# Optimization experiments

Hardware: AMD Instinct MI355X
Metric: run time of the kernel (lower is better)

The kernel has to match this reference:

```python
import jax, jax.numpy as jnp
import numpy as np

DIM = 32
NUM_FEATURES = 16
NUM_GRAPHS = 64
EDGE_HID = 64


def setup_inputs() -> dict:
    key = jax.random.key(0)
    ks = jax.random.split(key, 24)
    N, E = 25000, 250000
    p = lambda k, shape: (jax.random.normal(k, shape, dtype=jnp.float32) * 0.05)
    return {
        "x": jax.random.normal(ks[0], (N, NUM_FEATURES), dtype=jnp.float32),
        "edge_index": jax.random.randint(ks[1], (2, E), 0, N, dtype=jnp.int32),
        "edge_attr": jax.random.uniform(ks[2], (E, 5), dtype=jnp.float32),
        "batch": jnp.sort(jax.random.randint(ks[3], (N,), 0, NUM_GRAPHS, dtype=jnp.int32)),
        "lin0_w": p(ks[4], (NUM_FEATURES, DIM)),
        "lin0_b": p(ks[5], (DIM,)),
        "mlp_w1": p(ks[6], (5, EDGE_HID)),
        "mlp_b1": p(ks[7], (EDGE_HID,)),
        "mlp_w2": p(ks[8], (EDGE_HID, DIM * DIM)),
        "mlp_b2": p(ks[9], (DIM * DIM,)),
        "conv_bias": p(ks[10], (DIM,)),
        "gru_w_ih": p(ks[11], (3 * DIM, DIM)),
        "gru_w_hh": p(ks[12], (3 * DIM, DIM)),
        "gru_b_ih": p(ks[13], (3 * DIM,)),
        "gru_b_hh": p(ks[14], (3 * DIM,)),
        "lstm_w_ih": p(ks[15], (4 * DIM, 2 * DIM)),
        "lstm_w_hh": p(ks[16], (4 * DIM, DIM)),
        "lstm_b_ih": p(ks[17], (4 * DIM,)),
        "lstm_b_hh": p(ks[18], (4 * DIM,)),
    }


def reference(x, edge_index, edge_attr, batch, lin0_w, lin0_b, mlp_w1, mlp_b1,
              mlp_w2, mlp_b2, conv_bias, gru_w_ih, gru_w_hh, gru_b_ih, gru_b_hh,
              lstm_w_ih, lstm_w_hh, lstm_b_ih, lstm_b_hh):
    N = x.shape[0]
    src, dst = edge_index[0], edge_index[1]

    # lin0 + relu
    out = jax.nn.relu(x @ lin0_w + lin0_b)  # [N, D]
    h = out

    # edge MLP -> per-edge [D, D] weight matrices (edge_attr is loop-invariant)
    ew = jax.nn.relu(edge_attr @ mlp_w1 + mlp_b1) @ mlp_w2 + mlp_b2
    W = ew.reshape(-1, DIM, DIM)  # [E, D, D]

    deg = jax.ops.segment_sum(jnp.ones_like(dst, dtype=x.dtype), dst, num_segments=N)
    deg = jnp.maximum(deg, 1.0)[:, None]

    feat_last = out
    for _ in range(3):
        # NNConv: gather, per-edge matmul, scatter-mean, bias, relu
        msg = jnp.einsum('ei,eio->eo', out[src], W)  # [E, D]
        agg = jax.ops.segment_sum(msg, dst, num_segments=N) / deg
        m = jax.nn.relu(agg + conv_bias)
        # GRU step (torch GRU gate order r, z, n)
        gi = m @ gru_w_ih.T + gru_b_ih
        gh = h @ gru_w_hh.T + gru_b_hh
        ir, iz, inn = jnp.split(gi, 3, axis=-1)
        hr, hz, hn = jnp.split(gh, 3, axis=-1)
        r = jax.nn.sigmoid(ir + hr)
        z = jax.nn.sigmoid(iz + hz)
        n = jnp.tanh(inn + r * hn)
        h = (1.0 - z) * n + z * h
        out = h
        feat_last = out

    # Set2Set pooling (3 processing steps), LSTM input 2D hidden D
    B = NUM_GRAPHS
    q_star = jnp.zeros((B, 2 * DIM), dtype=x.dtype)
    hh = jnp.zeros((B, DIM), dtype=x.dtype)
    cc = jnp.zeros((B, DIM), dtype=x.dtype)
    for _ in range(3):
        gates = q_star @ lstm_w_ih.T + lstm_b_ih + hh @ lstm_w_hh.T + lstm_b_hh
        gi_, gf_, gg_, go_ = jnp.split(gates, 4, axis=-1)
        i_ = jax.nn.sigmoid(gi_)
        f_ = jax.nn.sigmoid(gf_)
        g_ = jnp.tanh(gg_)
        o_ = jax.nn.sigmoid(go_)
        cc = f_ * cc + i_ * g_
        hh = o_ * jnp.tanh(cc)
        q = hh  # [B, D]
        e = jnp.sum(out * q[batch], axis=-1)  # [N]
        emax = jax.ops.segment_max(e, batch, num_segments=B)
        e2 = jnp.exp(e - emax[batch])
        denom = jax.ops.segment_sum(e2, batch, num_segments=B)
        a = e2 / denom[batch]
        r_pool = jax.ops.segment_sum(a[:, None] * out, batch, num_segments=B)
        q_star = jnp.concatenate([q, r_pool], axis=-1)  # [B, 2D]

    return (q_star, feat_last)
```

## Files before the change

kernel.cpp:

```cpp
#include <hip/hip_runtime.h>
#include <hip/hip_fp16.h>

#define NFEAT 16
#define D 32
#define NB 64
#define TCOLS 2080
#define CHUNK 8
#define CPAD 16
#define KBN 16

static inline size_t align_up(size_t x, size_t a){ return (x + a - 1) & ~(a - 1); }

typedef _Float16 f16x2 __attribute__((ext_vector_type(2)));
typedef _Float16 f16x8 __attribute__((ext_vector_type(8)));
typedef float f32x4 __attribute__((ext_vector_type(4)));

__device__ inline unsigned int pk2(float a, float b){
  __half2 h = __floats2half2_rn(a, b);
  union { __half2 h; unsigned int u; } cv; cv.h = h; return cv.u;
}

__device__ inline float dot2(unsigned int a, unsigned int b, float c){
  union { unsigned int u; f16x2 h; } ua, ub; ua.u = a; ub.u = b;
#if __has_builtin(__builtin_amdgcn_fdot2)
  return __builtin_amdgcn_fdot2(ua.h, ub.h, c, false);
#else
  return c + (float)ua.h[0] * (float)ub.h[0] + (float)ua.h[1] * (float)ub.h[1];
#endif
}


__global__ __launch_bounds__(256) void kBuildMpk2(const float* __restrict__ w2,
                                                  const float* __restrict__ b2,
                                                  unsigned int* __restrict__ Mpk2){
  int idx = blockIdx.x * 256 + threadIdx.x;
  if (idx >= 130 * 64 * 4) return;
  int j2 = idx & 3;
  int l  = (idx >> 2) & 63;
  int c  = idx >> 8;
  int col = c * 16 + (l & 15);
  int h = col >> 5, o = col & 31;
  int ke = (l >> 4) * 8 + 2 * j2;
  float f0, f1;
  if (h < 64){
    f0 = w2[h * 1024 + ke * 32 + o];
    f1 = w2[h * 1024 + (ke + 1) * 32 + o];
  } else {
    f0 = b2[ke * 32 + o];
    f1 = b2[(ke + 1) * 32 + o];
  }
  Mpk2[idx] = pk2(f0, f1);
}

__global__ __launch_bounds__(256) void kLin0(const float* __restrict__ x,
                                             const float* __restrict__ w,
                                             const float* __restrict__ b,
                                             float* __restrict__ feat, int N){
  int idx = blockIdx.x * 256 + threadIdx.x;
  int u = idx >> 5, o = idx & 31;
  if (u >= N) return;
  float acc = b[o];
#pragma unroll
  for (int i = 0; i < NFEAT; i++) acc += x[(size_t)u * NFEAT + i] * w[i * 32 + o];
  feat[idx] = fmaxf(acc, 0.f);
}

__global__ __launch_bounds__(256) void kCountRank(const int* __restrict__ ei,
                                                  int* __restrict__ cnt_src,
                                                  int* __restrict__ cnt_dst,
                                                  int* __restrict__ rs,
                                                  int* __restrict__ rd, int E){
  int e = blockIdx.x * 256 + threadIdx.x;
  if (e >= E) return;
  int s = ei[e], d = ei[E + e];
  rs[e] = atomicAdd(&cnt_src[(size_t)s * CPAD], 1);
  rd[e] = atomicAdd(&cnt_dst[(size_t)d * CPAD], 1);
}

__global__ __launch_bounds__(256) void kScanA(const int* __restrict__ cnt_src,
                                              const int* __restrict__ cnt_dst,
                                              int* __restrict__ src_off,
                                              int* __restrict__ dst_off,
                                              int* __restrict__ bsum,
                                              float* __restrict__ deg,
                                              int N, int NT){
  int y = blockIdx.y;
  const int* cnt = y ? cnt_dst : cnt_src;
  int* off = y ? dst_off : src_off;
  int t = threadIdx.x;
  int i = blockIdx.x * 256 + t;
  int c = (i < N) ? cnt[(size_t)i * CPAD] : 0;
  if (y && i < N) deg[i] = (float)max(c, 1);
  __shared__ int sh[256];
  sh[t] = c; __syncthreads();
  for (int d = 1; d < 256; d <<= 1){
    int v = (t >= d) ? sh[t - d] : 0;
    __syncthreads();
    sh[t] += v;
    __syncthreads();
  }
  if (i < N) off[i] = sh[t] - c;
  if (t == 255) bsum[y * NT + blockIdx.x] = sh[255];
}

__global__ __launch_bounds__(256) void kScanB(int* __restrict__ bsum,
                                              const int* __restrict__ batch,
                                              int* __restrict__ boff,
                                              int* __restrict__ src_off,
                                              int* __restrict__ dst_off,
                                              int N, int NT, int B, int E){
  int t = threadIdx.x;
  __shared__ int sh[256];
  for (int y = 0; y < 2; y++){
    int v = (t < NT) ? bsum[y * NT + t] : 0;
    sh[t] = v; __syncthreads();
    for (int d = 1; d < 256; d <<= 1){
      int u = (t >= d) ? sh[t - d] : 0;
      __syncthreads();
      sh[t] += u;
      __syncthreads();
    }
    if (t < NT) bsum[y * NT + t] = sh[t] - v;
    __syncthreads();
  }
  if (t <= B){
    int lo = 0, hi = N;
    while (lo < hi){ int mid = (lo + hi) >> 1; if (batch[mid] < t) lo = mid + 1; else hi = mid; }
    boff[t] = lo;
  }
  if (t == 0){ src_off[N] = E; dst_off[N] = E; }
}

__global__ __launch_bounds__(256) void kScanC(int* __restrict__ src_off,
                                              int* __restrict__ dst_off,
                                              const int* __restrict__ bsum,
                                              int N, int NT){
  int y = blockIdx.y;
  int i = blockIdx.x * 256 + threadIdx.x;
  if (i < N) (y ? dst_off : src_off)[i] += bsum[y * NT + blockIdx.x];
}

__global__ __launch_bounds__(256) void kPlace(const int* __restrict__ ei,
                                              const int* __restrict__ src_off,
                                              const int* __restrict__ dst_off,
                                              const int* __restrict__ rs,
                                              const int* __restrict__ rd,
                                              int* __restrict__ so_eid,
                                              int* __restrict__ s2d, int E){
  int e = blockIdx.x * 256 + threadIdx.x;
  if (e >= E) return;
  int s = ei[e], d = ei[E + e];
  int ps = src_off[s] + rs[e];
  so_eid[ps] = e;
  s2d[ps] = dst_off[d] + rd[e];
}

__global__ __launch_bounds__(256) void kEdgeMLPpk(const float* __restrict__ ea,
                                                  const float* __restrict__ w1,
                                                  const float* __restrict__ b1,
                                                  const int* __restrict__ so_eid,
                                                  unsigned int* __restrict__ apk, int E){
  int idx = blockIdx.x * 256 + threadIdx.x;
  int j = idx >> 5, h2 = idx & 31;
  if (j >= E) return;
  int e = so_eid[j];
  const float* eap = ea + (size_t)e * 5;
  float q0 = eap[0], q1 = eap[1], q2 = eap[2], q3 = eap[3], q4 = eap[4];
  int h = 2 * h2;
  float lo = b1[h]     + q0 * w1[h]       + q1 * w1[64 + h]     + q2 * w1[128 + h]
                       + q3 * w1[192 + h] + q4 * w1[256 + h];
  float hi = b1[h + 1] + q0 * w1[h + 1]   + q1 * w1[64 + h + 1] + q2 * w1[128 + h + 1]
                       + q3 * w1[192 + h + 1] + q4 * w1[256 + h + 1];
  apk[(size_t)j * 32 + h2] = pk2(fmaxf(lo, 0.f), fmaxf(hi, 0.f));
}

__global__ __launch_bounds__(256, 4) void kTA(const float* __restrict__ feat,
                                              const uint4* __restrict__ Mpk2,
                                              const int* __restrict__ s2d,
                                              const unsigned int* __restrict__ apk,
                                              const int* __restrict__ src_off,
                                              float* __restrict__ msg,
                                              int N){
  __shared__ unsigned int Tp[CHUNK * 1024];
  __shared__ float bias_l[CHUNK][33];
  int tid = threadIdx.x;
  int c0 = blockIdx.x * CHUNK;
  int c1 = min(c0 + CHUNK, N);
  int nvalid = c1 - c0;
  int w = tid >> 6, l = tid & 63;
  int m = l & 15, q = l >> 4;

  {
    int nodeA = c0 + m;
    if (nodeA > c1 - 1) nodeA = c1 - 1;
    const float* fr = feat + (size_t)nodeA * 32 + q * 8;
    float4 fa = *(const float4*)fr;
    float4 fb = *(const float4*)(fr + 4);
    union { uint4 u; f16x8 h; } A;
    A.u.x = pk2(fa.x, fa.y); A.u.y = pk2(fa.z, fa.w);
    A.u.z = pk2(fb.x, fb.y); A.u.w = pk2(fb.z, fb.w);

    for (int job = w; job < 65; job += 4){
      int cE, cO, s = 0;
      if (job < 64){ int t = job >> 1; s = job & 1; cE = 4 * t + s; cO = 4 * t + 2 + s; }
      else { cE = 128; cO = 129; }
      union { uint4 u; f16x8 h; } BE, BO;
      BE.u = Mpk2[cE * 64 + l];
      BO.u = Mpk2[cO * 64 + l];
      f32x4 z = {0.f, 0.f, 0.f, 0.f};
      f32x4 dE = __builtin_amdgcn_mfma_f32_16x16x32_f16(A.h, BE.h, z, 0, 0, 0);
      f32x4 dO = __builtin_amdgcn_mfma_f32_16x16x32_f16(A.h, BO.h, z, 0, 0, 0);
      if (job < 64){
        int t = job >> 1;
        int o = s * 16 + m;
        int sw = (((t >> 2) ^ (m & 7)) << 2) | (t & 3);
#pragma unroll
        for (int r = 0; r < 4; r++){
          int nn = q * 4 + r;
          if (nn < nvalid) Tp[nn * 1024 + o * 32 + sw] = pk2(dE[r], dO[r]);
        }
      } else {
#pragma unroll
        for (int r = 0; r < 4; r++){
          int nn = q * 4 + r;
          if (nn < nvalid){
            bias_l[nn][m]      = dE[r];
            bias_l[nn][16 + m] = dO[r];
          }
        }
      }
    }
  }
  __syncthreads();

  for (int un = 0; un < 2; un++){
    int u = w * 2 + un;
    if (u >= nvalid) continue;
    int su = src_off[c0 + u], eu = src_off[c0 + u + 1];
    if (su >= eu) continue;
    const uint4* tb = (const uint4*)(Tp + u * 1024);
    union { uint4 u4; f16x8 h; } B00, B01, B10, B11;
    B00.u4 = tb[m * 8 + (q ^ (m & 7))];
    B10.u4 = tb[m * 8 + ((4 + q) ^ (m & 7))];
    B01.u4 = tb[(16 + m) * 8 + (q ^ (m & 7))];
    B11.u4 = tb[(16 + m) * 8 + ((4 + q) ^ (m & 7))];
    float b0 = bias_l[u][m], b1 = bias_l[u][16 + m];
    for (int jt = su; jt < eu; jt += 16){
      union { uint4 u4; f16x8 h; } A0, A1;
      const uint4* arow = (const uint4*)(apk + (size_t)(jt + m) * 32);
      A0.u4 = arow[q];
      A1.u4 = arow[4 + q];
      f32x4 z = {0.f, 0.f, 0.f, 0.f};
      f32x4 D0 = __builtin_amdgcn_mfma_f32_16x16x32_f16(A0.h, B00.h, z, 0, 0, 0);
      D0 = __builtin_amdgcn_mfma_f32_16x16x32_f16(A1.h, B10.h, D0, 0, 0, 0);
      f32x4 D1 = __builtin_amdgcn_mfma_f32_16x16x32_f16(A0.h, B01.h, z, 0, 0, 0);
      D1 = __builtin_amdgcn_mfma_f32_16x16x32_f16(A1.h, B11.h, D1, 0, 0, 0);
#pragma unroll
      for (int r = 0; r < 4; r++){
        int e = jt + q * 4 + r;
        if (e < eu){
          int dpos = s2d[e];
          msg[(size_t)dpos * 32 + m]      = D0[r] + b0;
          msg[(size_t)dpos * 32 + 16 + m] = D1[r] + b1;
        }
      }
    }
  }
}

__global__ __launch_bounds__(256) void kB(const float* __restrict__ msg,
                                          const int* __restrict__ dst_off,
                                          const float* __restrict__ deg,
                                          const float* __restrict__ feat_in,
                                          float* __restrict__ feat_out,
                                          float* __restrict__ out2,
                                          const float* __restrict__ Wih,
                                          const float* __restrict__ Whh,
                                          const float* __restrict__ bih,
                                          const float* __restrict__ bhh,
                                          const float* __restrict__ cbias, int N){
  __shared__ unsigned int wihpk[96][17], whhpk[96][17];
  __shared__ float bi[96], bh[96], cb[32];
  __shared__ unsigned int mshpk[8][17], hshpk[8][17];
  int tid = threadIdx.x;
  for (int k = tid; k < 96 * 16; k += 256){
    int g = k >> 4, q2 = k & 15;
    wihpk[g][q2] = pk2(Wih[g * 32 + 2 * q2], Wih[g * 32 + 2 * q2 + 1]);
    whhpk[g][q2] = pk2(Whh[g * 32 + 2 * q2], Whh[g * 32 + 2 * q2 + 1]);
  }
  if (tid < 96){ bi[tid] = bih[tid]; bh[tid] = bhh[tid]; }
  if (tid < 32) cb[tid] = cbias[tid];
  __syncthreads();
  int s = tid >> 5, o = tid & 31;
  for (int g8 = 0; g8 < KBN / 8; g8++){
    int v = blockIdx.x * KBN + g8 * 8 + s;
    if (v < N){
      int lo = dst_off[v], hi = dst_off[v + 1];
      float h = feat_in[(size_t)v * 32 + o];
      float a0 = 0.f, a1 = 0.f, a2 = 0.f, a3 = 0.f;
      int k = lo;
      for (; k + 3 < hi; k += 4){
        a0 += msg[(size_t)(k + 0) * 32 + o];
        a1 += msg[(size_t)(k + 1) * 32 + o];
        a2 += msg[(size_t)(k + 2) * 32 + o];
        a3 += msg[(size_t)(k + 3) * 32 + o];
      }
      for (; k < hi; k++) a0 += msg[(size_t)k * 32 + o];
      float acc = (a0 + a1) + (a2 + a3);
      float m = fmaxf(acc / deg[v] + cb[o], 0.f);
      float m1 = __shfl_down(m, 1);
      float h1 = __shfl_down(h, 1);
      if (!(o & 1)){
        mshpk[s][o >> 1] = pk2(m, m1);
        hshpk[s][o >> 1] = pk2(h, h1);
      }
      float gr = bi[o], gz = bi[32 + o], gn = bi[64 + o];
      float hr = bh[o], hz = bh[32 + o], hn = bh[64 + o];
#pragma unroll
      for (int q2 = 0; q2 < 16; q2++){
        unsigned int mq = mshpk[s][q2], hq = hshpk[s][q2];
        gr = dot2(mq, wihpk[o][q2], gr);
        gz = dot2(mq, wihpk[32 + o][q2], gz);
        gn = dot2(mq, wihpk[64 + o][q2], gn);
        hr = dot2(hq, whhpk[o][q2], hr);
        hz = dot2(hq, whhpk[32 + o][q2], hz);
        hn = dot2(hq, whhpk[64 + o][q2], hn);
      }
      float r = 1.f / (1.f + expf(-(gr + hr)));
      float z = 1.f / (1.f + expf(-(gz + hz)));
      float n = tanhf(gn + r * hn);
      float val = (1.f - z) * n + z * h;
      feat_out[(size_t)v * 32 + o] = val;
      if (out2) out2[(size_t)v * 32 + o] = val;
    }
  }
}

__global__ __launch_bounds__(256) void kS2S(const float* __restrict__ feat,
                                            const int* __restrict__ boff,
                                            const float* __restrict__ Wih,
                                            const float* __restrict__ Whh,
                                            const float* __restrict__ bih,
                                            const float* __restrict__ bhh,
                                            float* __restrict__ e_buf,
                                            float* __restrict__ out){
  int b = blockIdx.x;
  __shared__ float WihL[128][65];
  __shared__ float WhhL[128][33];
  __shared__ float qs[64], hst[32], cst[32], garr[128];
  __shared__ float wred[4];
  __shared__ float part[8][33];
  int tid = threadIdx.x;
  for (int k = tid; k < 128 * 64; k += 256) WihL[k >> 6][k & 63] = Wih[k];
  for (int k = tid; k < 128 * 32; k += 256) WhhL[k >> 5][k & 31] = Whh[k];
  if (tid < 64) qs[tid] = 0.f;
  if (tid < 32){ hst[tid] = 0.f; cst[tid] = 0.f; }
  __syncthreads();
  int lo = boff[b], hi = boff[b + 1];
  int sub = tid >> 5, o = tid & 31;
  for (int step = 0; step < 3; step++){
    if (tid < 128){
      float acc = bih[tid] + bhh[tid];
#pragma unroll 8
      for (int j = 0; j < 64; j++) acc += qs[j] * WihL[tid][j];
#pragma unroll 8
      for (int j = 0; j < 32; j++) acc += hst[j] * WhhL[tid][j];
      garr[tid] = acc;
    }
    __syncthreads();
    if (tid < 32){
      float iv = 1.f / (1.f + expf(-garr[tid]));
      float fv = 1.f / (1.f + expf(-garr[32 + tid]));
      float gv = tanhf(garr[64 + tid]);
      float ov = 1.f / (1.f + expf(-garr[96 + tid]));
      float c = fv * cst[tid] + iv * gv;
      cst[tid] = c;
      float hv = ov * tanhf(c);
      hst[tid] = hv;
      qs[tid] = hv;
    }
    __syncthreads();
    float mx = -1e30f;
    for (int i = lo + tid; i < hi; i += 256){
      const float* fr = feat + (size_t)i * 32;
      float acc = 0.f;
#pragma unroll
      for (int c4 = 0; c4 < 8; c4++){
        float4 f = *(const float4*)(fr + c4 * 4);
        acc += f.x * hst[c4 * 4] + f.y * hst[c4 * 4 + 1]
             + f.z * hst[c4 * 4 + 2] + f.w * hst[c4 * 4 + 3];
      }
      e_buf[i] = acc;
      mx = fmaxf(mx, acc);
    }
#pragma unroll
    for (int d2 = 32; d2; d2 >>= 1) mx = fmaxf(mx, __shfl_xor(mx, d2, 64));
    if ((tid & 63) == 0) wred[tid >> 6] = mx;
    __syncthreads();
    mx = fmaxf(fmaxf(wred[0], wred[1]), fmaxf(wred[2], wred[3]));
    __syncthreads();
    float sm = 0.f;
    for (int i = lo + tid; i < hi; i += 256){
      float w2 = expf(e_buf[i] - mx);
      e_buf[i] = w2;
      sm += w2;
    }
#pragma unroll
    for (int d2 = 32; d2; d2 >>= 1) sm += __shfl_xor(sm, d2, 64);
    if ((tid & 63) == 0) wred[tid >> 6] = sm;
    __syncthreads();
    float denom = fmaxf(wred[0] + wred[1] + wred[2] + wred[3], 1e-30f);
    float a0 = 0.f, a1 = 0.f, a2 = 0.f, a3 = 0.f;
    int i = lo + sub;
    for (; i + 24 < hi; i += 32){
      a0 += e_buf[i]      * feat[(size_t)i * 32 + o];
      a1 += e_buf[i + 8]  * feat[(size_t)(i + 8) * 32 + o];
      a2 += e_buf[i + 16] * feat[(size_t)(i + 16) * 32 + o];
      a3 += e_buf[i + 24] * feat[(size_t)(i + 24) * 32 + o];
    }
    for (; i < hi; i += 8) a0 += e_buf[i] * feat[(size_t)i * 32 + o];
    part[sub][o] = (a0 + a1) + (a2 + a3);
    __syncthreads();
    if (tid < 32){
      float r2 = 0.f;
#pragma unroll
      for (int s2 = 0; s2 < 8; s2++) r2 += part[s2][tid];
      qs[32 + tid] = r2 / denom;
    }
    __syncthreads();
  }
  if (tid < 64) out[b * 64 + tid] = qs[tid];
}


extern "C" void kernel_launch(void* const* d_in, const int* in_sizes, int n_in,
                              void* d_out, int out_size, void* d_ws, size_t ws_size,
                              hipStream_t stream){
  (void)n_in; (void)out_size; (void)ws_size;
  const float* x        = (const float*)d_in[0];
  const int*   ei       = (const int*)  d_in[1];
  const float* eattr    = (const float*)d_in[2];
  const int*   batch    = (const int*)  d_in[3];
  const float* lin0_w   = (const float*)d_in[4];
  const float* lin0_b   = (const float*)d_in[5];
  const float* mlp_w1   = (const float*)d_in[6];
  const float* mlp_b1   = (const float*)d_in[7];
  const float* mlp_w2   = (const float*)d_in[8];
  const float* mlp_b2   = (const float*)d_in[9];
  const float* conv_b   = (const float*)d_in[10];
  const float* gru_wih  = (const float*)d_in[11];
  const float* gru_whh  = (const float*)d_in[12];
  const float* gru_bih  = (const float*)d_in[13];
  const float* gru_bhh  = (const float*)d_in[14];
  const float* lstm_wih = (const float*)d_in[15];
  const float* lstm_whh = (const float*)d_in[16];
  const float* lstm_bih = (const float*)d_in[17];
  const float* lstm_bhh = (const float*)d_in[18];

  int N = in_sizes[0] / NFEAT;
  int E = in_sizes[1] / 2;
  int NT = (N + 255) / 256;

  char* ws = (char*)d_ws;
  size_t off = 0;
  auto alloc = [&](size_t bytes) -> char* {
    char* p = ws + off;
    off = align_up(off + bytes, 256);
    return p;
  };

  float* feat0  = (float*)alloc((size_t)N * D * 4);
  float* feat1  = (float*)alloc((size_t)N * D * 4);
  float* msg    = (float*)alloc((size_t)E * D * 4);
  unsigned int* Mpk2 = (unsigned int*)alloc((size_t)130 * 64 * 4 * 4);
  unsigned int* apk = (unsigned int*)alloc((size_t)E * 32 * 4 + 4096);
  float* e_buf  = (float*)alloc((size_t)N * 4);
  float* deg    = (float*)alloc((size_t)N * 4);
  int* cnt_src  = (int*)alloc((size_t)N * CPAD * 4);
  int* cnt_dst  = (int*)alloc((size_t)N * CPAD * 4);
  int* rs       = (int*)alloc((size_t)E * 4);
  int* rd       = (int*)alloc((size_t)E * 4);
  int* src_off  = (int*)alloc((size_t)(N + 1) * 4);
  int* dst_off  = (int*)alloc((size_t)(N + 1) * 4);
  int* boff     = (int*)alloc((size_t)(NB + 1) * 4);
  int* bsum     = (int*)alloc((size_t)2 * NT * 4);
  int* so_eid   = (int*)alloc((size_t)E * 4);
  int* s2d      = (int*)alloc((size_t)E * 4 + 256);

  (void)hipMemsetAsync(cnt_src, 0, (size_t)N * CPAD * 4 * 2, stream);

  kBuildMpk2<<<(130 * 64 * 4 + 255) / 256, 256, 0, stream>>>(mlp_w2, mlp_b2, Mpk2);
  kLin0<<<(N * 32 + 255) / 256, 256, 0, stream>>>(x, lin0_w, lin0_b, feat0, N);
  kCountRank<<<(E + 255) / 256, 256, 0, stream>>>(ei, cnt_src, cnt_dst, rs, rd, E);
  {
    dim3 gA(NT, 2);
    kScanA<<<gA, 256, 0, stream>>>(cnt_src, cnt_dst, src_off, dst_off, bsum, deg, N, NT);
    kScanB<<<1, 256, 0, stream>>>(bsum, batch, boff, src_off, dst_off, N, NT, NB, E);
    kScanC<<<gA, 256, 0, stream>>>(src_off, dst_off, bsum, N, NT);
  }
  kPlace<<<(E + 255) / 256, 256, 0, stream>>>(ei, src_off, dst_off, rs, rd,
                                              so_eid, s2d, E);
  kEdgeMLPpk<<<((size_t)E * 32 + 255) / 256, 256, 0, stream>>>(eattr, mlp_w1, mlp_b1,
                                                               so_eid, apk, E);

  int blocksTA = (N + CHUNK - 1) / CHUNK;
  float* fcur = feat0;
  float* fnext = feat1;
  for (int t = 0; t < 3; t++){
    kTA<<<blocksTA, 256, 0, stream>>>(fcur, (const uint4*)Mpk2, s2d, apk,
                                      src_off, msg, N);
    float* out2 = (t == 2) ? ((float*)d_out + NB * 64) : nullptr;
    kB<<<(N + KBN - 1) / KBN, 256, 0, stream>>>(msg, dst_off, deg, fcur, fnext, out2,
                                                gru_wih, gru_whh, gru_bih, gru_bhh,
                                                conv_b, N);
    float* tmp = fcur; fcur = fnext; fnext = tmp;
  }

  kS2S<<<NB, 256, 0, stream>>>(fcur, boff, lstm_wih, lstm_whh, lstm_bih, lstm_bhh,
                               e_buf, (float*)d_out);
}
```

Baseline: 309.3 us.

## Store per-edge messages as packed fp16 and unroll the T-build job loop

The per-edge message buffer changes from fp32 to packed fp16 pairs. kTA writes one 32-bit word per lane holding outputs m and m+16, and kB reads them back using a dot2 against a selector vector to pick the right half. This halves the scattered write and gathered read traffic on the E×32 message buffer, which is the dominant memory stream in each of the three conv iterations. Separately, the job loop that builds the per-node T matrices is restructured into a fixed 16-iteration unrolled loop per wave, with the bias job handled by wave 3. The fp16 storage of messages adds rounding error before the mean aggregation.

```diff
diff --git a/kernel.cpp b/kernel.cpp
--- a/kernel.cpp
+++ b/kernel.cpp
@@ -179,7 +179,7 @@
                                               const int* __restrict__ s2d,
                                               const unsigned int* __restrict__ apk,
                                               const int* __restrict__ src_off,
-                                              float* __restrict__ msg,
+                                              unsigned int* __restrict__ msg16,
                                               int N){
   __shared__ unsigned int Tp[CHUNK * 1024];
   __shared__ float bias_l[CHUNK][33];
@@ -200,33 +200,38 @@
     A.u.x = pk2(fa.x, fa.y); A.u.y = pk2(fa.z, fa.w);
     A.u.z = pk2(fb.x, fb.y); A.u.w = pk2(fb.z, fb.w);
 
-    for (int job = w; job < 65; job += 4){
-      int cE, cO, s = 0;
-      if (job < 64){ int t = job >> 1; s = job & 1; cE = 4 * t + s; cO = 4 * t + 2 + s; }
-      else { cE = 128; cO = 129; }
+#pragma unroll 4
+    for (int jj2 = 0; jj2 < 16; jj2++){
+      int job = w * 16 + jj2;
+      int t = job >> 1, s = job & 1;
+      int cE = 4 * t + s, cO = 4 * t + 2 + s;
       union { uint4 u; f16x8 h; } BE, BO;
       BE.u = Mpk2[cE * 64 + l];
       BO.u = Mpk2[cO * 64 + l];
       f32x4 z = {0.f, 0.f, 0.f, 0.f};
       f32x4 dE = __builtin_amdgcn_mfma_f32_16x16x32_f16(A.h, BE.h, z, 0, 0, 0);
       f32x4 dO = __builtin_amdgcn_mfma_f32_16x16x32_f16(A.h, BO.h, z, 0, 0, 0);
-      if (job < 64){
-        int t = job >> 1;
-        int o = s * 16 + m;
-        int sw = (((t >> 2) ^ (m & 7)) << 2) | (t & 3);
-#pragma unroll
-        for (int r = 0; r < 4; r++){
-          int nn = q * 4 + r;
-          if (nn < nvalid) Tp[nn * 1024 + o * 32 + sw] = pk2(dE[r], dO[r]);
-        }
-      } else {
-#pragma unroll
-        for (int r = 0; r < 4; r++){
-          int nn = q * 4 + r;
-          if (nn < nvalid){
-            bias_l[nn][m]      = dE[r];
-            bias_l[nn][16 + m] = dO[r];
-          }
+      int o = s * 16 + m;
+      int sw = (((t >> 2) ^ (m & 7)) << 2) | (t & 3);
+#pragma unroll
+      for (int r = 0; r < 4; r++){
+        int nn = q * 4 + r;
+        if (nn < nvalid) Tp[nn * 1024 + o * 32 + sw] = pk2(dE[r], dO[r]);
+      }
+    }
+    if (w == 3){
+      union { uint4 u; f16x8 h; } BE, BO;
+      BE.u = Mpk2[128 * 64 + l];
+      BO.u = Mpk2[129 * 64 + l];
+      f32x4 z = {0.f, 0.f, 0.f, 0.f};
+      f32x4 dE = __builtin_amdgcn_mfma_f32_16x16x32_f16(A.h, BE.h, z, 0, 0, 0);
+      f32x4 dO = __builtin_amdgcn_mfma_f32_16x16x32_f16(A.h, BO.h, z, 0, 0, 0);
+#pragma unroll
+      for (int r = 0; r < 4; r++){
+        int nn = q * 4 + r;
+        if (nn < nvalid){
+          bias_l[nn][m]      = dE[r];
+          bias_l[nn][16 + m] = dO[r];
         }
       }
     }
@@ -259,16 +264,14 @@
       for (int r = 0; r < 4; r++){
         int e = jt + q * 4 + r;
         if (e < eu){
-          int dpos = s2d[e];
-          msg[(size_t)dpos * 32 + m]      = D0[r] + b0;
-          msg[(size_t)dpos * 32 + 16 + m] = D1[r] + b1;
+          msg16[(size_t)s2d[e] * 16 + m] = pk2(D0[r] + b0, D1[r] + b1);
         }
       }
     }
   }
 }
 
-__global__ __launch_bounds__(256) void kB(const float* __restrict__ msg,
+__global__ __launch_bounds__(256) void kB(const unsigned int* __restrict__ msg16,
                                           const int* __restrict__ dst_off,
                                           const float* __restrict__ deg,
                                           const float* __restrict__ feat_in,
@@ -292,6 +295,8 @@
   if (tid < 32) cb[tid] = cbias[tid];
   __syncthreads();
   int s = tid >> 5, o = tid & 31;
+  unsigned int sel = (o < 16) ? pk2(1.f, 0.f) : pk2(0.f, 1.f);
+  int w16 = o & 15;
   for (int g8 = 0; g8 < KBN / 8; g8++){
     int v = blockIdx.x * KBN + g8 * 8 + s;
     if (v < N){
@@ -300,12 +305,12 @@
       float a0 = 0.f, a1 = 0.f, a2 = 0.f, a3 = 0.f;
       int k = lo;
       for (; k + 3 < hi; k += 4){
-        a0 += msg[(size_t)(k + 0) * 32 + o];
-        a1 += msg[(size_t)(k + 1) * 32 + o];
-        a2 += msg[(size_t)(k + 2) * 32 + o];
-        a3 += msg[(size_t)(k + 3) * 32 + o];
-      }
-      for (; k < hi; k++) a0 += msg[(size_t)k * 32 + o];
+        a0 = dot2(msg16[(size_t)(k + 0) * 16 + w16], sel, a0);
+        a1 = dot2(msg16[(size_t)(k + 1) * 16 + w16], sel, a1);
+        a2 = dot2(msg16[(size_t)(k + 2) * 16 + w16], sel, a2);
+        a3 = dot2(msg16[(size_t)(k + 3) * 16 + w16], sel, a3);
+      }
+      for (; k < hi; k++) a0 = dot2(msg16[(size_t)k * 16 + w16], sel, a0);
       float acc = (a0 + a1) + (a2 + a3);
       float m = fmaxf(acc / deg[v] + cb[o], 0.f);
       float m1 = __shfl_down(m, 1);
@@ -471,7 +476,7 @@
 
   float* feat0  = (float*)alloc((size_t)N * D * 4);
   float* feat1  = (float*)alloc((size_t)N * D * 4);
-  float* msg    = (float*)alloc((size_t)E * D * 4);
+  unsigned int* msg16 = (unsigned int*)alloc((size_t)E * 16 * 4);
   unsigned int* Mpk2 = (unsigned int*)alloc((size_t)130 * 64 * 4 * 4);
   unsigned int* apk = (unsigned int*)alloc((size_t)E * 32 * 4 + 4096);
   float* e_buf  = (float*)alloc((size_t)N * 4);
@@ -508,9 +513,9 @@
   float* fnext = feat1;
   for (int t = 0; t < 3; t++){
     kTA<<<blocksTA, 256, 0, stream>>>(fcur, (const uint4*)Mpk2, s2d, apk,
-                                      src_off, msg, N);
+                                      src_off, msg16, N);
     float* out2 = (t == 2) ? ((float*)d_out + NB * 64) : nullptr;
-    kB<<<(N + KBN - 1) / KBN, 256, 0, stream>>>(msg, dst_off, deg, fcur, fnext, out2,
+    kB<<<(N + KBN - 1) / KBN, 256, 0, stream>>>(msg16, dst_off, deg, fcur, fnext, out2,
                                                 gru_wih, gru_whh, gru_bih, gru_bhh,
                                                 conv_b, N);
     float* tmp = fcur; fcur = fnext; fnext = tmp;
```

Result: faster. 298.7 us (-3.4%).
